# Optimization experiments

Measured on AMD Instinct MI355X. Metric: run time of the kernel, lower is better.

The kernel has to match this reference:

```python
import jax, jax.numpy as jnp
import numpy as np
from jax import lax

STRIDE = (1, 1)  # module init arg; stride slicing of the spectrum


def next_pow2(k: int) -> int:
    return 1 << (int(k) - 1).bit_length()


def setup_inputs() -> dict:
    key = jax.random.key(0)
    k1, k2, k3 = jax.random.split(key, 3)
    B, H, W, C, F = 16, 128, 128, 16, 32
    image = jax.random.normal(k1, (B, H, W, C), dtype=jnp.float32)
    # kernel shape per module: (2*H/stride_h, W/stride_w + 1, features, C)
    kh, kw = 2 * H // STRIDE[0], W // STRIDE[1] + 1
    kernel_real = jax.random.normal(k2, (kh, kw, F, C), dtype=jnp.float32)
    kernel_imag = jax.random.normal(k3, (kh, kw, F, C), dtype=jnp.float32)
    bias = jnp.zeros((F,), dtype=jnp.float32)
    return {"image": image, "kernel_real": kernel_real,
            "kernel_imag": kernel_imag, "bias": bias}


def reference(image, kernel_real, kernel_imag, bias):
    kernel = kernel_real + 1j * kernel_imag  # complex64 [kh, kw, F, C]
    B, H, W, C = image.shape
    padded = (2 * H - 1, 2 * W - 1)                       # "full" conv extent
    fast = (next_pow2(padded[0]), next_pow2(padded[1]))    # FFT-friendly pad
    fast_strided = (next_pow2(kernel.shape[0]), next_pow2(kernel.shape[1]))
    # rfft2 over spatial axes -> [B, fast_h, fast_w//2+1, C]
    F_img = jnp.fft.rfft2(image, s=fast, axes=(1, 2))
    F_img = F_img[:, ::STRIDE[0], ::STRIDE[1]]
    # channel contraction in Fourier space (vmap+sum in original == einsum)
    out_f = jnp.einsum('bhwc,hwfc->bhwf', F_img, kernel)
    # back to real space: [B, fast_strided_h, fast_strided_w, F]
    conv = jnp.fft.irfft2(out_f, s=fast_strided, axes=(1, 2))
    conv = conv + bias
    # crop to full-conv extent, then center-crop to "same" shape
    conv = conv[:, :padded[0], :padded[1], :]
    sh = (padded[0] - H) // 2
    sw = (padded[1] - W) // 2
    return lax.slice(conv, (0, sh, sw, 0),
                     (B, sh + H, sw + W, conv.shape[-1]))
```

## Files before the change

kernel.cpp:

```cpp
#include <hip/hip_runtime.h>
#include <math.h>


constexpr int Bn = 16, Cc = 16, Ff = 32, Hh = 128, Ww = 128, Nn = 256, WH = 129;

#define DEVINL __device__ __forceinline__
DEVINL float2 f2(float a, float b) { return make_float2(a, b); }
DEVINL float2 cmul(float2 a, float2 b) { return f2(a.x * b.x - a.y * b.y, a.x * b.y + a.y * b.x); }

DEVINL unsigned short f2bf(float f) { unsigned u = __float_as_uint(f); return (unsigned short)((u + 0x8000u) >> 16); }
DEVINL float bf2f(unsigned short h) { return __uint_as_float(((unsigned)h) << 16); }
DEVINL unsigned packbf(float a, float b) { return (unsigned)f2bf(a) | ((unsigned)f2bf(b) << 16); }
DEVINL unsigned pk2u(float2 z) { return packbf(z.x, z.y); }
DEVINL ushort2 pk2(float2 z) { return make_ushort2(f2bf(z.x), f2bf(z.y)); }
DEVINL float2 up2(ushort2 u) { return f2(bf2f(u.x), bf2f(u.y)); }
DEVINL float2 upu(unsigned u) { return f2(bf2f((unsigned short)(u & 0xffffu)), bf2f((unsigned short)(u >> 16))); }

typedef __attribute__((ext_vector_type(8))) short short8;
typedef __attribute__((ext_vector_type(4))) float f32x4;
typedef __attribute__((ext_vector_type(4))) float fv4;

DEVINL int IDX(int r, int e) { return r * 256 + ((e + r) & 255); }

template<int SGN>
DEVINL void fft16r(float2 v[16]) {
  float2 t;
#define SW(a,b) { t = v[a]; v[a] = v[b]; v[b] = t; }
  SW(1, 8) SW(2, 4) SW(3, 12) SW(5, 10) SW(7, 14) SW(11, 13)
#undef SW
  const float C1 = 0.92387953251128674f, C2 = 0.70710678118654752f, C3 = 0.38268343236508977f;
  const float Ct[8] = {1.f, C1, C2, C3, 0.f, -C3, -C2, -C1};
  const float St[8] = {0.f, C3, C2, C1, 1.f, C1, C2, C3};
#pragma unroll
  for (int len = 2; len <= 16; len <<= 1) {
    const int half = len >> 1, ts = 16 / len;
#pragma unroll
    for (int i = 0; i < 16; i += len) {
#pragma unroll
      for (int j = 0; j < half; ++j) {
        const float wr = Ct[j * ts];
        const float wi = (SGN > 0) ? St[j * ts] : -St[j * ts];
        float2 b = v[i + j + half];
        float2 tt = f2(wr * b.x - wi * b.y, wr * b.y + wi * b.x);
        float2 a = v[i + j];
        v[i + j]        = f2(a.x + tt.x, a.y + tt.y);
        v[i + j + half] = f2(a.x - tt.x, a.y - tt.y);
      }
    }
  }
}

template<int SGN>
DEVINL void twiddle16(float2 v[16], int t) {
  const float unit = (SGN > 0) ? 0.024543692606170259f : -0.024543692606170259f;
  float sb, cb;
  __sincosf(unit * (float)t, &sb, &cb);
  float2 W[16];
  W[1] = f2(cb, sb);
#pragma unroll
  for (int k = 2; k < 16; ++k) W[k] = cmul(W[k >> 1], W[k - (k >> 1)]);
#pragma unroll
  for (int k = 1; k < 16; ++k) v[k] = cmul(v[k], W[k]);
}

template<int SGN>
DEVINL void fft256_mid(float2 v[16], float2* __restrict__ lds, int r, int t) {
  fft16r<SGN>(v);
  twiddle16<SGN>(v, t);
#pragma unroll
  for (int k = 0; k < 16; ++k) lds[IDX(r, t * 16 + ((k + t) & 15))] = v[k];
#pragma unroll
  for (int n2 = 0; n2 < 16; ++n2) v[n2] = lds[IDX(r, n2 * 16 + ((t + n2) & 15))];
  fft16r<SGN>(v);
}

__global__ __launch_bounds__(512) void k1_rowfft(const float* __restrict__ img, ushort2* __restrict__ R) {
  __shared__ float2 lds[32 * 256];
  const int tid = threadIdx.x, s = tid >> 4, t = tid & 15;
  const int y0 = blockIdx.x * 2, b = blockIdx.y;
  const float4* ip4 = (const float4*)(img + ((size_t)(b * Hh + y0) * Ww) * Cc);
  for (int i = tid; i < 2 * Ww * 4; i += 512) {
    int yb = i >> 9, rem = i & 511, x = rem >> 2, j = rem & 3;
    float4 u = ip4[(size_t)yb * 512 + rem];
    lds[IDX(yb * 16 + 4 * j + 0, x)] = f2(u.x, 0.f);
    lds[IDX(yb * 16 + 4 * j + 1, x)] = f2(u.y, 0.f);
    lds[IDX(yb * 16 + 4 * j + 2, x)] = f2(u.z, 0.f);
    lds[IDX(yb * 16 + 4 * j + 3, x)] = f2(u.w, 0.f);
  }
  __syncthreads();
  float2 v[16];
#pragma unroll
  for (int j = 0; j < 8; ++j) v[j] = lds[IDX(s, t + 16 * j)];
#pragma unroll
  for (int j = 8; j < 16; ++j) v[j] = f2(0.f, 0.f);
  fft256_mid<-1>(v, lds, s, t);
#pragma unroll
  for (int k = 0; k < 8; ++k) lds[IDX(s, t + 16 * k)] = v[k];
  if (t == 0) lds[IDX(s, 128)] = v[8];
  __syncthreads();
  ushort2* rp = R + ((size_t)b * WH * Hh + y0) * Cc;
  for (int i = tid; i < WH * 32; i += 512) {
    int w = i >> 5, row = i & 31;
    rp[(size_t)w * Hh * Cc + row] = pk2(lds[IDX(row, w)]);
  }
}

__global__ __launch_bounds__(512) void k2_colfft(const ushort2* __restrict__ R, ushort2* __restrict__ Fimg) {
  __shared__ float2 lds[32 * 256];
  const int tid = threadIdx.x, s = tid >> 4, t = tid & 15;
  const int w = blockIdx.x, b0 = blockIdx.y * 2;
  const uint4* rp4 = (const uint4*)(R + ((size_t)(b0 * WH + w) * Hh) * Cc);
  const size_t bstride4 = (size_t)WH * Hh * Cc / 4;
  for (int i = tid; i < 2 * Hh * 4; i += 512) {
    int bb = i >> 9, rem = i & 511, y = rem >> 2, j = rem & 3;
    uint4 u = rp4[(size_t)bb * bstride4 + rem];
    lds[IDX(bb * 16 + 4 * j + 0, y)] = upu(u.x);
    lds[IDX(bb * 16 + 4 * j + 1, y)] = upu(u.y);
    lds[IDX(bb * 16 + 4 * j + 2, y)] = upu(u.z);
    lds[IDX(bb * 16 + 4 * j + 3, y)] = upu(u.w);
  }
  __syncthreads();
  float2 v[16];
#pragma unroll
  for (int j = 0; j < 8; ++j) v[j] = lds[IDX(s, t + 16 * j)];
#pragma unroll
  for (int j = 8; j < 16; ++j) v[j] = f2(0.f, 0.f);
  fft256_mid<-1>(v, lds, s, t);
#pragma unroll
  for (int k2 = 0; k2 < 16; ++k2) lds[IDX(s, t + 16 * k2)] = v[k2];
  __syncthreads();
  ushort2* fp = Fimg + (size_t)w * 256 + b0 * 16;
  for (int i = tid; i < Nn * 32; i += 512) {
    int h = i >> 5, row = i & 31;
    fp[(size_t)h * WH * 256 + row] = pk2(lds[IDX(row, h)]);
  }
}

constexpr int K3PTS = 2;
__global__ __launch_bounds__(128) void k3_mul(const ushort2* __restrict__ Fimg, const float* __restrict__ Kr,
                                              const float* __restrict__ Ki, ushort2* __restrict__ OF) {
  const int tid = threadIdx.x;
  const int wv = tid >> 6, ln = tid & 63;
  const int w = blockIdx.x, h0 = blockIdx.y * (2 * K3PTS) + wv * K3PTS;
  const int q = ln >> 4, fq = ln & 15, m0 = q & 1;
  const bool hi = (q >= 2);
  const int sh = hi ? 16 : 0;
  const unsigned negmask = hi ? 0x80008000u : 0u;

  union U { unsigned u[4]; short8 s; };

  uint4  a0[2], a1[2];
  float4 kA[2], kB[2], kC[2], kD[2];
  float4 iA[2], iB[2], iC[2], iD[2];

  auto load = [&](int g, int p) {
    const size_t base = (size_t)(h0 + g) * WH + w;
    const uint4* ap = (const uint4*)(Fimg + base * 256);
    a0[p] = ap[fq * 4 + 2 * m0];
    a1[p] = ap[fq * 4 + 2 * m0 + 1];
    const float* kb = Kr + base * 512 + fq * 16 + 8 * m0;
    const float* ib = Ki + base * 512 + fq * 16 + 8 * m0;
    kA[p] = *(const float4*)kb;          kB[p] = *(const float4*)(kb + 4);
    kC[p] = *(const float4*)(kb + 256);  kD[p] = *(const float4*)(kb + 260);
    iA[p] = *(const float4*)ib;          iB[p] = *(const float4*)(ib + 4);
    iC[p] = *(const float4*)(ib + 256);  iD[p] = *(const float4*)(ib + 260);
  };

  auto compute = [&](int g, int p) {
    U ua;
    ua.u[0] = ((a0[p].x >> sh) & 0xffffu) | (((a0[p].y >> sh) & 0xffffu) << 16);
    ua.u[1] = ((a0[p].z >> sh) & 0xffffu) | (((a0[p].w >> sh) & 0xffffu) << 16);
    ua.u[2] = ((a1[p].x >> sh) & 0xffffu) | (((a1[p].y >> sh) & 0xffffu) << 16);
    ua.u[3] = ((a1[p].z >> sh) & 0xffffu) | (((a1[p].w >> sh) & 0xffffu) << 16);

    U ubr0, ubi0, ubr1, ubi1;
    {
      unsigned krP[4] = { packbf(kA[p].x, kA[p].y), packbf(kA[p].z, kA[p].w),
                          packbf(kB[p].x, kB[p].y), packbf(kB[p].z, kB[p].w) };
      unsigned kiP[4] = { packbf(iA[p].x, iA[p].y), packbf(iA[p].z, iA[p].w),
                          packbf(iB[p].x, iB[p].y), packbf(iB[p].z, iB[p].w) };
#pragma unroll
      for (int j = 0; j < 4; ++j) {
        ubr0.u[j] = (hi ? kiP[j] : krP[j]) ^ negmask;
        ubi0.u[j] = hi ? krP[j] : kiP[j];
      }
    }
    {
      unsigned krP[4] = { packbf(kC[p].x, kC[p].y), packbf(kC[p].z, kC[p].w),
                          packbf(kD[p].x, kD[p].y), packbf(kD[p].z, kD[p].w) };
      unsigned kiP[4] = { packbf(iC[p].x, iC[p].y), packbf(iC[p].z, iC[p].w),
                          packbf(iD[p].x, iD[p].y), packbf(iD[p].z, iD[p].w) };
#pragma unroll
      for (int j = 0; j < 4; ++j) {
        ubr1.u[j] = (hi ? kiP[j] : krP[j]) ^ negmask;
        ubi1.u[j] = hi ? krP[j] : kiP[j];
      }
    }

    f32x4 aR0 = {0.f, 0.f, 0.f, 0.f}, aI0 = {0.f, 0.f, 0.f, 0.f};
    f32x4 aR1 = {0.f, 0.f, 0.f, 0.f}, aI1 = {0.f, 0.f, 0.f, 0.f};
    aR0 = __builtin_amdgcn_mfma_f32_16x16x32_bf16(ua.s, ubr0.s, aR0, 0, 0, 0);
    aI0 = __builtin_amdgcn_mfma_f32_16x16x32_bf16(ua.s, ubi0.s, aI0, 0, 0, 0);
    aR1 = __builtin_amdgcn_mfma_f32_16x16x32_bf16(ua.s, ubr1.s, aR1, 0, 0, 0);
    aI1 = __builtin_amdgcn_mfma_f32_16x16x32_bf16(ua.s, ubi1.s, aI1, 0, 0, 0);

    uint2* op = (uint2*)(OF + ((size_t)w * 256 + (h0 + g)) * 512);
#pragma unroll
    for (int reg = 0; reg < 4; ++reg)
      op[(4 * q + reg) * 16 + fq] = make_uint2(packbf(aR0[reg], aI0[reg]),
                                               packbf(aR1[reg], aI1[reg]));
  };

  load(0, 0);
  load(1, 1);
  __builtin_amdgcn_sched_barrier(0);
  compute(0, 0);
  compute(1, 1);
}

__global__ __launch_bounds__(512) void k4_colifft(const ushort2* __restrict__ OF, ushort2* __restrict__ T) {
  __shared__ float2 lds[32 * 256];
  const int tid = threadIdx.x, s = tid >> 4, t = tid & 15;
  const int bidx = blockIdx.x;
  const int b = bidx & 15, w = bidx >> 4;
  const int j8 = tid & 7;
  const uint4* ofp4 = (const uint4*)OF + (size_t)w * 32768;
  for (int i = tid; i < Nn * 8; i += 512) {
    int h = i >> 3, j = i & 7;
    uint4 u = ofp4[(size_t)h * 128 + b * 8 + j];
    lds[IDX(2 * j, h)]      = upu(u.x);
    lds[IDX(2 * j + 16, h)] = upu(u.y);
    lds[IDX(2 * j + 1, h)]  = upu(u.z);
    lds[IDX(2 * j + 17, h)] = upu(u.w);
  }
  __syncthreads();
  float2 v[16];
#pragma unroll
  for (int j = 0; j < 16; ++j) v[j] = lds[IDX(s, t + 16 * j)];
  fft256_mid<1>(v, lds, s, t);
#pragma unroll
  for (int k2 = 3; k2 < 12; ++k2) lds[IDX(s, t + 16 * k2)] = v[k2];
  __syncthreads();
  uint4* tp4 = (uint4*)T + ((size_t)b * Hh * WH + w) * 8;
  for (int i = tid; i < Hh * 8; i += 512) {
    int yp = i >> 3, j = i & 7;
    uint4 st;
    st.x = pk2u(lds[IDX(4 * j + 0, 63 + yp)]);
    st.y = pk2u(lds[IDX(4 * j + 1, 63 + yp)]);
    st.z = pk2u(lds[IDX(4 * j + 2, 63 + yp)]);
    st.w = pk2u(lds[IDX(4 * j + 3, 63 + yp)]);
    tp4[(size_t)yp * WH * 8 + j] = st;
  }
  (void)j8;
}

__global__ __launch_bounds__(512) void k5_rowifft(const ushort2* __restrict__ T, const float* __restrict__ bias,
                                                  float* __restrict__ out) {
  __shared__ float2 lds[32 * 256];
  const int tid = threadIdx.x, s = tid >> 4, t = tid & 15;
  const int yp = blockIdx.x, b = blockIdx.y;
  const uint4* tp4 = (const uint4*)T + ((size_t)(b * Hh + yp) * WH) * 8;
  for (int i = tid; i < WH * 8; i += 512) {
    int w = i >> 3, j = i & 7;
    uint4 u = tp4[(size_t)w * 8 + j];
    lds[IDX(4 * j + 0, w)] = upu(u.x);
    lds[IDX(4 * j + 1, w)] = upu(u.y);
    lds[IDX(4 * j + 2, w)] = upu(u.z);
    lds[IDX(4 * j + 3, w)] = upu(u.w);
  }
  __syncthreads();
  float2 v[16];
#pragma unroll
  for (int n1 = 0; n1 < 16; ++n1) {
    const int c = t + 16 * n1;
    if (c <= 128) v[n1] = lds[IDX(s, c)];
    else { float2 z = lds[IDX(s, 256 - c)]; v[n1] = f2(z.x, -z.y); }
  }
  fft256_mid<1>(v, lds, s, t);
#pragma unroll
  for (int k2 = 3; k2 < 12; ++k2) lds[IDX(s, t + 16 * k2)] = v[k2];
  __syncthreads();
  const float sc = 1.f / 65536.f;
  const int j8 = tid & 7;
  const float bv0 = bias[4 * j8 + 0], bv1 = bias[4 * j8 + 1];
  const float bv2 = bias[4 * j8 + 2], bv3 = bias[4 * j8 + 3];
  fv4* op = (fv4*)(out + ((size_t)(b * Hh + yp) * Ww) * Ff);
  for (int i = tid; i < Ww * 8; i += 512) {
    int x = i >> 3, j = i & 7;
    fv4 st;
    st.x = lds[IDX(4 * j + 0, 63 + x)].x * sc + bv0;
    st.y = lds[IDX(4 * j + 1, 63 + x)].x * sc + bv1;
    st.z = lds[IDX(4 * j + 2, 63 + x)].x * sc + bv2;
    st.w = lds[IDX(4 * j + 3, 63 + x)].x * sc + bv3;
    __builtin_nontemporal_store(st, &op[(size_t)x * 8 + j]);
  }
}

extern "C" void kernel_launch(void* const* d_in, const int* in_sizes, int n_in,
                              void* d_out, int out_size, void* d_ws, size_t ws_size,
                              hipStream_t stream) {
  const float* img  = (const float*)d_in[0];
  const float* kr   = (const float*)d_in[1];
  const float* ki   = (const float*)d_in[2];
  const float* bias = (const float*)d_in[3];
  float* out = (float*)d_out;

  char* ws = (char*)d_ws;
  const size_t szF = (size_t)Nn * WH * Bn * Cc * sizeof(float2);
  ushort2* Fimg = (ushort2*)ws;
  ushort2* T    = (ushort2*)ws;
  ushort2* OF   = (ushort2*)(ws + szF);
  ushort2* R    = (ushort2*)(ws + szF);

  k1_rowfft <<<dim3(Hh / 2, Bn),  512, 0, stream>>>(img, R);
  k2_colfft <<<dim3(WH, Bn / 2),  512, 0, stream>>>(R, Fimg);
  k3_mul    <<<dim3(WH, 64),      128, 0, stream>>>(Fimg, kr, ki, OF);
  k4_colifft<<<dim3(WH * Bn),     512, 0, stream>>>(OF, T);
  k5_rowifft<<<dim3(Hh, Bn),      512, 0, stream>>>(T, bias, out);
}
```

Baseline: 133.9 us.

## Fuse spectral channel contraction with column inverse FFT in shared memory

Merges the Fourier-domain multiply kernel and the column inverse FFT kernel into one kernel. Each block handles four batches for one frequency column, keeps the product spectrum in a 128KB LDS buffer as packed bf16, and runs the 256-point inverse FFT in place before writing T. This removes the OF intermediate round trip through global memory and one launch. In exchange, the MFMA tiles are only a quarter used (the other 12 batch rows are zero-padded), each kernel tile is reloaded across the 4 batch groups, grid parallelism drops to 516 blocks, and the large LDS footprint limits occupancy.

Result: slower. 239.9 us (+79.2%).

```diff
diff --git a/kernel.cpp b/kernel.cpp
--- a/kernel.cpp
+++ b/kernel.cpp
@@ -21,6 +21,7 @@
 typedef __attribute__((ext_vector_type(4))) float fv4;
 
 DEVINL int IDX(int r, int e) { return r * 256 + ((e + r) & 255); }
+#define OFSID(e, r) ((e) * 128 + (((r) + (e)) & 127))
 
 template<int SGN>
 DEVINL void fft16r(float2 v[16]) {
@@ -136,49 +137,49 @@
   }
 }
 
-constexpr int K3PTS = 2;
-__global__ __launch_bounds__(128) void k3_mul(const ushort2* __restrict__ Fimg, const float* __restrict__ Kr,
-                                              const float* __restrict__ Ki, ushort2* __restrict__ OF) {
+__global__ __launch_bounds__(512) void k34_mulifft(const ushort2* __restrict__ Fimg,
+                                                   const float* __restrict__ Kr,
+                                                   const float* __restrict__ Ki,
+                                                   ushort2* __restrict__ T) {
+  __shared__ unsigned ofs[256 * 128];
   const int tid = threadIdx.x;
+  const int bg = blockIdx.x, w = blockIdx.y;
+  const int b0 = bg * 4;
   const int wv = tid >> 6, ln = tid & 63;
-  const int w = blockIdx.x, h0 = blockIdx.y * (2 * K3PTS) + wv * K3PTS;
   const int q = ln >> 4, fq = ln & 15, m0 = q & 1;
   const bool hi = (q >= 2);
   const int sh = hi ? 16 : 0;
   const unsigned negmask = hi ? 0x80008000u : 0u;
-
   union U { unsigned u[4]; short8 s; };
 
-  uint4  a0[2], a1[2];
-  float4 kA[2], kB[2], kC[2], kD[2];
-  float4 iA[2], iB[2], iC[2], iD[2];
-
-  auto load = [&](int g, int p) {
-    const size_t base = (size_t)(h0 + g) * WH + w;
-    const uint4* ap = (const uint4*)(Fimg + base * 256);
-    a0[p] = ap[fq * 4 + 2 * m0];
-    a1[p] = ap[fq * 4 + 2 * m0 + 1];
+  for (int i = 0; i < 32; ++i) {
+    const int h = wv + 8 * i;
+    const size_t base = (size_t)h * WH + w;
+    uint4 a0 = make_uint4(0, 0, 0, 0), a1 = make_uint4(0, 0, 0, 0);
+    if (fq < 4) {
+      const uint4* ap = (const uint4*)(Fimg + base * 256);
+      a0 = ap[(b0 + fq) * 4 + 2 * m0];
+      a1 = ap[(b0 + fq) * 4 + 2 * m0 + 1];
+    }
     const float* kb = Kr + base * 512 + fq * 16 + 8 * m0;
     const float* ib = Ki + base * 512 + fq * 16 + 8 * m0;
-    kA[p] = *(const float4*)kb;          kB[p] = *(const float4*)(kb + 4);
-    kC[p] = *(const float4*)(kb + 256);  kD[p] = *(const float4*)(kb + 260);
-    iA[p] = *(const float4*)ib;          iB[p] = *(const float4*)(ib + 4);
-    iC[p] = *(const float4*)(ib + 256);  iD[p] = *(const float4*)(ib + 260);
-  };
-
-  auto compute = [&](int g, int p) {
+    const float4 kr00 = *(const float4*)kb;          const float4 kr01 = *(const float4*)(kb + 4);
+    const float4 kr10 = *(const float4*)(kb + 256);  const float4 kr11 = *(const float4*)(kb + 260);
+    const float4 ki00 = *(const float4*)ib;          const float4 ki01 = *(const float4*)(ib + 4);
+    const float4 ki10 = *(const float4*)(ib + 256);  const float4 ki11 = *(const float4*)(ib + 260);
+
     U ua;
-    ua.u[0] = ((a0[p].x >> sh) & 0xffffu) | (((a0[p].y >> sh) & 0xffffu) << 16);
-    ua.u[1] = ((a0[p].z >> sh) & 0xffffu) | (((a0[p].w >> sh) & 0xffffu) << 16);
-    ua.u[2] = ((a1[p].x >> sh) & 0xffffu) | (((a1[p].y >> sh) & 0xffffu) << 16);
-    ua.u[3] = ((a1[p].z >> sh) & 0xffffu) | (((a1[p].w >> sh) & 0xffffu) << 16);
+    ua.u[0] = ((a0.x >> sh) & 0xffffu) | (((a0.y >> sh) & 0xffffu) << 16);
+    ua.u[1] = ((a0.z >> sh) & 0xffffu) | (((a0.w >> sh) & 0xffffu) << 16);
+    ua.u[2] = ((a1.x >> sh) & 0xffffu) | (((a1.y >> sh) & 0xffffu) << 16);
+    ua.u[3] = ((a1.z >> sh) & 0xffffu) | (((a1.w >> sh) & 0xffffu) << 16);
 
     U ubr0, ubi0, ubr1, ubi1;
     {
-      unsigned krP[4] = { packbf(kA[p].x, kA[p].y), packbf(kA[p].z, kA[p].w),
-                          packbf(kB[p].x, kB[p].y), packbf(kB[p].z, kB[p].w) };
-      unsigned kiP[4] = { packbf(iA[p].x, iA[p].y), packbf(iA[p].z, iA[p].w),
-                          packbf(iB[p].x, iB[p].y), packbf(iB[p].z, iB[p].w) };
+      unsigned krP[4] = { packbf(kr00.x, kr00.y), packbf(kr00.z, kr00.w),
+                          packbf(kr01.x, kr01.y), packbf(kr01.z, kr01.w) };
+      unsigned kiP[4] = { packbf(ki00.x, ki00.y), packbf(ki00.z, ki00.w),
+                          packbf(ki01.x, ki01.y), packbf(ki01.z, ki01.w) };
 #pragma unroll
       for (int j = 0; j < 4; ++j) {
         ubr0.u[j] = (hi ? kiP[j] : krP[j]) ^ negmask;
@@ -186,10 +187,10 @@
       }
     }
     {
-      unsigned krP[4] = { packbf(kC[p].x, kC[p].y), packbf(kC[p].z, kC[p].w),
-                          packbf(kD[p].x, kD[p].y), packbf(kD[p].z, kD[p].w) };
-      unsigned kiP[4] = { packbf(iC[p].x, iC[p].y), packbf(iC[p].z, iC[p].w),
-                          packbf(iD[p].x, iD[p].y), packbf(iD[p].z, iD[p].w) };
+      unsigned krP[4] = { packbf(kr10.x, kr10.y), packbf(kr10.z, kr10.w),
+                          packbf(kr11.x, kr11.y), packbf(kr11.z, kr11.w) };
+      unsigned kiP[4] = { packbf(ki10.x, ki10.y), packbf(ki10.z, ki10.w),
+                          packbf(ki11.x, ki11.y), packbf(ki11.z, ki11.w) };
 #pragma unroll
       for (int j = 0; j < 4; ++j) {
         ubr1.u[j] = (hi ? kiP[j] : krP[j]) ^ negmask;
@@ -204,54 +205,46 @@
     aR1 = __builtin_amdgcn_mfma_f32_16x16x32_bf16(ua.s, ubr1.s, aR1, 0, 0, 0);
     aI1 = __builtin_amdgcn_mfma_f32_16x16x32_bf16(ua.s, ubi1.s, aI1, 0, 0, 0);
 
-    uint2* op = (uint2*)(OF + ((size_t)w * 256 + (h0 + g)) * 512);
-#pragma unroll
-    for (int reg = 0; reg < 4; ++reg)
-      op[(4 * q + reg) * 16 + fq] = make_uint2(packbf(aR0[reg], aI0[reg]),
-                                               packbf(aR1[reg], aI1[reg]));
-  };
-
-  load(0, 0);
-  load(1, 1);
-  __builtin_amdgcn_sched_barrier(0);
-  compute(0, 0);
-  compute(1, 1);
-}
-
-__global__ __launch_bounds__(512) void k4_colifft(const ushort2* __restrict__ OF, ushort2* __restrict__ T) {
-  __shared__ float2 lds[32 * 256];
-  const int tid = threadIdx.x, s = tid >> 4, t = tid & 15;
-  const int bidx = blockIdx.x;
-  const int b = bidx & 15, w = bidx >> 4;
-  const int j8 = tid & 7;
-  const uint4* ofp4 = (const uint4*)OF + (size_t)w * 32768;
-  for (int i = tid; i < Nn * 8; i += 512) {
-    int h = i >> 3, j = i & 7;
-    uint4 u = ofp4[(size_t)h * 128 + b * 8 + j];
-    lds[IDX(2 * j, h)]      = upu(u.x);
-    lds[IDX(2 * j + 16, h)] = upu(u.y);
-    lds[IDX(2 * j + 1, h)]  = upu(u.z);
-    lds[IDX(2 * j + 17, h)] = upu(u.w);
-  }
-  __syncthreads();
-  float2 v[16];
-#pragma unroll
-  for (int j = 0; j < 16; ++j) v[j] = lds[IDX(s, t + 16 * j)];
-  fft256_mid<1>(v, lds, s, t);
-#pragma unroll
-  for (int k2 = 3; k2 < 12; ++k2) lds[IDX(s, t + 16 * k2)] = v[k2];
-  __syncthreads();
-  uint4* tp4 = (uint4*)T + ((size_t)b * Hh * WH + w) * 8;
-  for (int i = tid; i < Hh * 8; i += 512) {
-    int yp = i >> 3, j = i & 7;
+    if (q == 0) {
+#pragma unroll
+      for (int reg = 0; reg < 4; ++reg) {
+        ofs[OFSID(h, reg * 32 + fq)]      = packbf(aR0[reg], aI0[reg]);
+        ofs[OFSID(h, reg * 32 + fq + 16)] = packbf(aR1[reg], aI1[reg]);
+      }
+    }
+  }
+  __syncthreads();
+
+  const int s = tid >> 4, t = tid & 15;
+#pragma unroll
+  for (int round = 0; round < 4; ++round) {
+    const int r = s + 32 * round;
+    float2 v[16];
+#pragma unroll
+    for (int j = 0; j < 16; ++j) v[j] = upu(ofs[OFSID(t + 16 * j, r)]);
+    fft16r<1>(v);
+    twiddle16<1>(v, t);
+#pragma unroll
+    for (int k = 0; k < 16; ++k) ofs[OFSID(t * 16 + ((k + t) & 15), r)] = pk2u(v[k]);
+#pragma unroll
+    for (int n2 = 0; n2 < 16; ++n2) v[n2] = upu(ofs[OFSID(n2 * 16 + ((t + n2) & 15), r)]);
+    fft16r<1>(v);
+#pragma unroll
+    for (int k2 = 3; k2 < 12; ++k2) ofs[OFSID(t + 16 * k2, r)] = pk2u(v[k2]);
+  }
+  __syncthreads();
+
+  uint4* tpu4 = (uint4*)T;
+  for (int i = tid; i < 128 * 32; i += 512) {
+    int yp = i >> 5, rr = i & 31;
+    int bb = rr >> 3, j = rr & 7;
     uint4 st;
-    st.x = pk2u(lds[IDX(4 * j + 0, 63 + yp)]);
-    st.y = pk2u(lds[IDX(4 * j + 1, 63 + yp)]);
-    st.z = pk2u(lds[IDX(4 * j + 2, 63 + yp)]);
-    st.w = pk2u(lds[IDX(4 * j + 3, 63 + yp)]);
-    tp4[(size_t)yp * WH * 8 + j] = st;
-  }
-  (void)j8;
+    st.x = ofs[OFSID(63 + yp, bb * 32 + 4 * j + 0)];
+    st.y = ofs[OFSID(63 + yp, bb * 32 + 4 * j + 1)];
+    st.z = ofs[OFSID(63 + yp, bb * 32 + 4 * j + 2)];
+    st.w = ofs[OFSID(63 + yp, bb * 32 + 4 * j + 3)];
+    tpu4[((size_t)(b0 + bb) * Hh * WH + (size_t)yp * WH + w) * 8 + j] = st;
+  }
 }
 
 __global__ __launch_bounds__(512) void k5_rowifft(const ushort2* __restrict__ T, const float* __restrict__ bias,
@@ -308,13 +301,11 @@
   char* ws = (char*)d_ws;
   const size_t szF = (size_t)Nn * WH * Bn * Cc * sizeof(float2);
   ushort2* Fimg = (ushort2*)ws;
-  ushort2* T    = (ushort2*)ws;
-  ushort2* OF   = (ushort2*)(ws + szF);
   ushort2* R    = (ushort2*)(ws + szF);
-
-  k1_rowfft <<<dim3(Hh / 2, Bn),  512, 0, stream>>>(img, R);
-  k2_colfft <<<dim3(WH, Bn / 2),  512, 0, stream>>>(R, Fimg);
-  k3_mul    <<<dim3(WH, 64),      128, 0, stream>>>(Fimg, kr, ki, OF);
-  k4_colifft<<<dim3(WH * Bn),     512, 0, stream>>>(OF, T);
-  k5_rowifft<<<dim3(Hh, Bn),      512, 0, stream>>>(T, bias, out);
-}
+  ushort2* T    = (ushort2*)(ws + szF);
+
+  k1_rowfft  <<<dim3(Hh / 2, Bn),  512, 0, stream>>>(img, R);
+  k2_colfft  <<<dim3(WH, Bn / 2),  512, 0, stream>>>(R, Fimg);
+  k34_mulifft<<<dim3(4, WH),       512, 0, stream>>>(Fimg, kr, ki, T);
+  k5_rowifft <<<dim3(Hh, Bn),      512, 0, stream>>>(T, bias, out);
+}
```
